# Kernel tuning notes

Measured on AMD Instinct MI355X. Metric: run time of the kernel, lower is better.

The kernel has to match this reference:

```python
import jax, jax.numpy as jnp
import numpy as np


def setup_inputs() -> dict:
    key = jax.random.key(0)
    ks = jax.random.split(key, 13)
    B, D, H, O = 4096, 2048, 3, 1  # batch, input_dim, hidden layer count, output_dim
    f32 = jnp.float32
    scale = 1.0 / np.sqrt(D)
    return {
        "x": jax.random.normal(ks[0], (B, D), f32),
        "w_mu_h": jax.random.normal(ks[1], (H, D, D), f32) * scale,
        "w_rho_h": jax.random.normal(ks[2], (H, D, D), f32) - 5.0,  # softplus(-5) ~ small std
        "b_mu_h": jax.random.normal(ks[3], (H, D), f32) * scale,
        "b_rho_h": jax.random.normal(ks[4], (H, D), f32) - 5.0,
        "w_mu_o": jax.random.normal(ks[5], (O, D), f32) * scale,
        "w_rho_o": jax.random.normal(ks[6], (O, D), f32) - 5.0,
        "b_mu_o": jax.random.normal(ks[7], (O,), f32) * scale,
        "b_rho_o": jax.random.normal(ks[8], (O,), f32) - 5.0,
        # reparameterization noise (torch.randn_like), passed explicitly for determinism
        "eps_w_h": jax.random.normal(ks[9], (H, D, D), f32),
        "eps_b_h": jax.random.normal(ks[10], (H, D), f32),
        "eps_w_o": jax.random.normal(ks[11], (O, D), f32),
        "eps_b_o": jax.random.normal(ks[12], (O,), f32),
    }


def _vlinear(x, w_mu, w_rho, b_mu, b_rho, eps_w, eps_b):
    # weight = mu + eps * softplus(rho); F.linear(x, W, b) = x @ W.T + b
    w = w_mu + eps_w * jax.nn.softplus(w_rho)
    b = b_mu + eps_b * jax.nn.softplus(b_rho)
    return x @ w.T + b


def reference(x, w_mu_h, w_rho_h, b_mu_h, b_rho_h,
              w_mu_o, w_rho_o, b_mu_o, b_rho_o,
              eps_w_h, eps_b_h, eps_w_o, eps_b_o):
    def step(h, p):
        wm, wr, bm, br, ew, eb = p
        h = jax.nn.relu(_vlinear(h, wm, wr, bm, br, ew, eb))
        return h, None

    h, _ = jax.lax.scan(step, x, (w_mu_h, w_rho_h, b_mu_h, b_rho_h, eps_w_h, eps_b_h))
    return _vlinear(h, w_mu_o, w_rho_o, b_mu_o, b_rho_o, eps_w_o, eps_b_o)
```

## Files before the change

### kernel.cpp

```cpp
#include <hip/hip_runtime.h>

#define BB 4096
#define DD 2048

typedef float f32x4 __attribute__((ext_vector_type(4)));
typedef __bf16 bf16x8 __attribute__((ext_vector_type(8)));

typedef __attribute__((address_space(1))) unsigned int gl_u32;
typedef __attribute__((address_space(3))) unsigned int lds_u32;

#define GLOAD_LDS16(gptr, sptr) \
  __builtin_amdgcn_global_load_lds((gl_u32*)(void*)(gptr), (lds_u32*)(sptr), 16, 0, 0)

#define SBAR_MEM() asm volatile("s_barrier" ::: "memory")
#define VMCNT(n)   asm volatile("s_waitcnt vmcnt(" #n ")" ::: "memory")
#define LGKMCNT0() asm volatile("s_waitcnt lgkmcnt(0)" ::: "memory")

__device__ __forceinline__ unsigned short f2bf(float f) {
  unsigned int u = __float_as_uint(f);
  u += 0x7fffu + ((u >> 16) & 1u);
  return (unsigned short)(u >> 16);
}

__device__ __forceinline__ float sp(float x) {
  float t = __expf(-fabsf(x));
  return fmaxf(x, 0.0f) + __logf(1.0f + t);
}

__device__ __forceinline__ void prep_w_vec4(
    const float* __restrict__ mu, const float* __restrict__ rho,
    const float* __restrict__ eps, unsigned short* __restrict__ Wh,
    long long i)
{
  float4 m = ((const float4*)mu)[i];
  float4 r = ((const float4*)rho)[i];
  float4 e = ((const float4*)eps)[i];
  ushort4 o;
  o.x = f2bf(m.x + e.x * sp(r.x));
  o.y = f2bf(m.y + e.y * sp(r.y));
  o.z = f2bf(m.z + e.z * sp(r.z));
  o.w = f2bf(m.w + e.w * sp(r.w));
  ((ushort4*)Wh)[i] = o;
}

__device__ __forceinline__ void prep_f32_vec4(
    const float* __restrict__ mu, const float* __restrict__ rho,
    const float* __restrict__ eps, float* __restrict__ out, long long i)
{
  float4 m = ((const float4*)mu)[i];
  float4 r = ((const float4*)rho)[i];
  float4 e = ((const float4*)eps)[i];
  float4 o;
  o.x = m.x + e.x * sp(r.x);
  o.y = m.y + e.y * sp(r.y);
  o.z = m.z + e.z * sp(r.z);
  o.w = m.w + e.w * sp(r.w);
  ((float4*)out)[i] = o;
}

__global__ __launch_bounds__(512) void prep0_kernel(
    const float* __restrict__ x,
    const float* __restrict__ wmuh, const float* __restrict__ wrhoh,
    const float* __restrict__ bmuh, const float* __restrict__ brhoh,
    const float* __restrict__ wmuo, const float* __restrict__ wrhoo,
    const float* __restrict__ epswh, const float* __restrict__ epsbh,
    const float* __restrict__ epswo,
    unsigned short* __restrict__ Wh, unsigned short* __restrict__ Xb,
    float* __restrict__ bh, float* __restrict__ wo)
{
  const int b = blockIdx.x;
  const int t = threadIdx.x;
  if (b < 1536) {
    long long base = (long long)b * 2048 + t;
    #pragma unroll
    for (int j = 0; j < 4; ++j)
      prep_w_vec4(wmuh, wrhoh, epswh, Wh, base + j * 512);
    return;
  }
  if (b < 2560) {
    long long base = (long long)(b - 1536) * 2048 + t;
    #pragma unroll
    for (int j = 0; j < 4; ++j) {
      float4 v = ((const float4*)x)[base + j * 512];
      ushort4 o;
      o.x = f2bf(v.x); o.y = f2bf(v.y); o.z = f2bf(v.z); o.w = f2bf(v.w);
      ((ushort4*)Xb)[base + j * 512] = o;
    }
    return;
  }
  #pragma unroll
  for (int j = 0; j < 3; ++j)
    prep_f32_vec4(bmuh, brhoh, epsbh, bh, j * 512 + t);
  prep_f32_vec4(wmuo, wrhoo, epswo, wo, t);
}

#define NGEMM 256

struct Coords256 { int m0, n0; int srow[4], sgc[4]; };

__device__ __forceinline__ Coords256 coords256(int id, int t) {
  Coords256 g;
  const int p = id & 7;
  const int i4 = id >> 3;
  const int mt = (p & 3) * 4 + (i4 & 3);
  const int nt = (p >> 2) * 8 + (i4 >> 2);
  g.m0 = mt * 256;
  g.n0 = nt * 128;
  #pragma unroll
  for (int i = 0; i < 4; ++i) {
    int c = i * 512 + t;
    g.srow[i] = c >> 3;
    g.sgc[i] = (c & 7) ^ (g.srow[i] & 7);
  }
  return g;
}

__device__ __forceinline__ void stage_half0(
    const unsigned short* __restrict__ A, const unsigned short* __restrict__ W,
    unsigned short* bufA, unsigned short* bufB,
    const Coords256& gc, int kt, int t)
{
  #pragma unroll
  for (int i = 0; i < 2; ++i) {
    int c = i * 512 + t;
    const unsigned short* ga = A + (size_t)(gc.m0 + gc.srow[i]) * DD + kt + gc.sgc[i] * 8;
    GLOAD_LDS16(ga, &bufA[c * 8]);
  }
  const unsigned short* gb = W + (size_t)(gc.n0 + gc.srow[0]) * DD + kt + gc.sgc[0] * 8;
  GLOAD_LDS16(gb, &bufB[t * 8]);
}

__device__ __forceinline__ void stage_half1(
    const unsigned short* __restrict__ A, const unsigned short* __restrict__ W,
    unsigned short* bufA, unsigned short* bufB,
    const Coords256& gc, int kt, int t)
{
  #pragma unroll
  for (int i = 2; i < 4; ++i) {
    int c = i * 512 + t;
    const unsigned short* ga = A + (size_t)(gc.m0 + gc.srow[i]) * DD + kt + gc.sgc[i] * 8;
    GLOAD_LDS16(ga, &bufA[c * 8]);
  }
  const unsigned short* gb = W + (size_t)(gc.n0 + gc.srow[1]) * DD + kt + gc.sgc[1] * 8;
  GLOAD_LDS16(gb, &bufB[(512 + t) * 8]);
}

__device__ __forceinline__ void compute_half(
    const unsigned short* bufA, const unsigned short* bufB, int s,
    int wm, int wn, int lq, int lr, f32x4 (&acc)[4][4])
{
  bf16x8 af[4], bfv[4];
  const int g = s * 4 + lq;
  const int go = (g ^ (lr & 7)) * 8;
  #pragma unroll
  for (int i = 0; i < 4; ++i) {
    int ra = wm * 64 + i * 16 + lr;
    af[i] = *(const bf16x8*)&bufA[ra * 64 + go];
  }
  #pragma unroll
  for (int j = 0; j < 4; ++j) {
    int rb = wn * 64 + j * 16 + lr;
    bfv[j] = *(const bf16x8*)&bufB[rb * 64 + go];
  }
  LGKMCNT0();
  __builtin_amdgcn_sched_barrier(0);
  __builtin_amdgcn_s_setprio(1);
  #pragma unroll
  for (int i = 0; i < 4; ++i)
    #pragma unroll
    for (int j = 0; j < 4; ++j)
      acc[i][j] = __builtin_amdgcn_mfma_f32_16x16x32_bf16(af[i], bfv[j], acc[i][j], 0, 0, 0);
  __builtin_amdgcn_s_setprio(0);
}

__device__ __forceinline__ void gemm_mainloop8p(
    const unsigned short* __restrict__ A, const unsigned short* __restrict__ W,
    unsigned short (*ldsA)[16384], unsigned short (*ldsB)[8192],
    const Coords256& gc, int t, f32x4 (&acc)[4][4])
{
  const int l = t & 63, lq = l >> 4, lr = l & 15;
  const int w = t >> 6, wm = w & 3, wn = w >> 2;
  unsigned short *a0 = ldsA[0], *a1 = ldsA[1], *a2 = ldsA[2];
  unsigned short *b0 = ldsB[0], *b1 = ldsB[1], *b2 = ldsB[2];
  stage_half0(A, W, a0, b0, gc, 0, t);
  stage_half1(A, W, a0, b0, gc, 0, t);
  stage_half0(A, W, a1, b1, gc, 64, t);
  stage_half1(A, W, a1, b1, gc, 64, t);
  for (int k = 0; k < 32; ++k) {
    if (k < 30) stage_half0(A, W, a2, b2, gc, (k + 2) * 64, t);
    __builtin_amdgcn_sched_barrier(0);
    if (k < 30)      { VMCNT(9); }
    else if (k == 30){ VMCNT(6); }
    else             { VMCNT(0); }
    SBAR_MEM();
    compute_half(a0, b0, 0, wm, wn, lq, lr, acc);
    SBAR_MEM();
    if (k < 30) stage_half1(A, W, a2, b2, gc, (k + 2) * 64, t);
    compute_half(a0, b0, 1, wm, wn, lq, lr, acc);
    SBAR_MEM();
    unsigned short* ta = a0; a0 = a1; a1 = a2; a2 = ta;
    unsigned short* tb = b0; b0 = b1; b1 = b2; b2 = tb;
  }
}

__device__ __forceinline__ void epilogue_store256(
    const Coords256& gc, int t, f32x4 (&acc)[4][4],
    const float* __restrict__ bias, unsigned short* __restrict__ C)
{
  const int l = t & 63, lq = l >> 4, lr = l & 15;
  const int w = t >> 6, wm = w & 3, wn = w >> 2;
  #pragma unroll
  for (int j = 0; j < 4; ++j) {
    int n = gc.n0 + wn * 64 + j * 16 + lr;
    float bv = bias[n];
    #pragma unroll
    for (int i = 0; i < 4; ++i) {
      int mbase = gc.m0 + wm * 64 + i * 16 + lq * 4;
      #pragma unroll
      for (int r = 0; r < 4; ++r) {
        float v = fmaxf(acc[i][j][r] + bv, 0.0f);
        C[(size_t)(mbase + r) * DD + n] = f2bf(v);
      }
    }
  }
}

__global__ __launch_bounds__(512, 2) void gemm_relu_kernel(
    const unsigned short* __restrict__ A,
    const unsigned short* __restrict__ W,
    const float* __restrict__ bias,
    unsigned short* __restrict__ C)
{
  __shared__ unsigned short ldsA[3][16384];
  __shared__ unsigned short ldsB[3][8192];
  const int t = threadIdx.x;
  Coords256 gc = coords256(blockIdx.x, t);
  f32x4 acc[4][4] = {};
  gemm_mainloop8p(A, W, ldsA, ldsB, gc, t, acc);
  epilogue_store256(gc, t, acc, bias, C);
}

__global__ __launch_bounds__(512, 2) void gemm_relu_dot_kernel(
    const unsigned short* __restrict__ A,
    const unsigned short* __restrict__ W,
    const float* __restrict__ bias,
    const float* __restrict__ wo,
    float* __restrict__ Pbuf)
{
  __shared__ unsigned short ldsA[3][16384];
  __shared__ unsigned short ldsB[3][8192];
  const int t = threadIdx.x;

  Coords256 gc = coords256(blockIdx.x, t);
  f32x4 acc[4][4] = {};
  gemm_mainloop8p(A, W, ldsA, ldsB, gc, t, acc);

  const int l = t & 63, lq = l >> 4, lr = l & 15;
  const int w = t >> 6, wm = w & 3, wn = w >> 2;

  float bv[4], wv[4];
  #pragma unroll
  for (int j = 0; j < 4; ++j) {
    int n = gc.n0 + wn * 64 + j * 16 + lr;
    bv[j] = bias[n];
    wv[j] = wo[n];
  }
  float partial[4][4];
  #pragma unroll
  for (int i = 0; i < 4; ++i)
    #pragma unroll
    for (int r = 0; r < 4; ++r) {
      float s = 0.0f;
      #pragma unroll
      for (int j = 0; j < 4; ++j)
        s += fmaxf(acc[i][j][r] + bv[j], 0.0f) * wv[j];
      partial[i][r] = s;
    }

  #pragma unroll
  for (int d = 1; d <= 8; d <<= 1)
    #pragma unroll
    for (int i = 0; i < 4; ++i)
      #pragma unroll
      for (int r = 0; r < 4; ++r)
        partial[i][r] += __shfl_xor(partial[i][r], d, 64);

  float* sRed = (float*)ldsA;
  if (lr == 0) {
    #pragma unroll
    for (int i = 0; i < 4; ++i)
      #pragma unroll
      for (int r = 0; r < 4; ++r) {
        int row = wm * 64 + i * 16 + lq * 4 + r;
        sRed[row * 2 + wn] = partial[i][r];
      }
  }
  __syncthreads();
  if (t < 256) {
    float s = sRed[t * 2 + 0] + sRed[t * 2 + 1];
    int nt = gc.n0 >> 7;
    Pbuf[nt * BB + gc.m0 + t] = s;
  }
}

__global__ __launch_bounds__(256) void reduce_out_kernel(
    const float* __restrict__ Pbuf,
    const float* __restrict__ bmuo, const float* __restrict__ brhoo,
    const float* __restrict__ epsbo,
    float* __restrict__ out)
{
  const int m = blockIdx.x * 256 + threadIdx.x;
  float s = bmuo[0] + epsbo[0] * sp(brhoo[0]);
  #pragma unroll
  for (int nt = 0; nt < 16; ++nt)
    s += Pbuf[nt * BB + m];
  out[m] = s;
}

extern "C" void kernel_launch(void* const* d_in, const int* in_sizes, int n_in,
                              void* d_out, int out_size, void* d_ws, size_t ws_size,
                              hipStream_t stream) {
  const float* x     = (const float*)d_in[0];
  const float* wmuh  = (const float*)d_in[1];
  const float* wrhoh = (const float*)d_in[2];
  const float* bmuh  = (const float*)d_in[3];
  const float* brhoh = (const float*)d_in[4];
  const float* wmuo  = (const float*)d_in[5];
  const float* wrhoo = (const float*)d_in[6];
  const float* bmuo  = (const float*)d_in[7];
  const float* brhoo = (const float*)d_in[8];
  const float* epswh = (const float*)d_in[9];
  const float* epsbh = (const float*)d_in[10];
  const float* epswo = (const float*)d_in[11];
  const float* epsbo = (const float*)d_in[12];

  char* ws = (char*)d_ws;
  unsigned short* Wh = (unsigned short*)(ws);
  unsigned short* Xb = (unsigned short*)(ws + 25165824);
  unsigned short* Ha = (unsigned short*)(ws + 25165824 + 16777216);
  unsigned short* Hb = (unsigned short*)(ws + 25165824 + 2 * 16777216);
  float* bh   = (float*)(ws + 25165824 + 3 * 16777216);
  float* wo   = (float*)(ws + 25165824 + 3 * 16777216 + 24576);
  float* Pbuf = (float*)(ws + 25165824 + 3 * 16777216 + 24576 + 8192);

  prep0_kernel<<<2561, 512, 0, stream>>>(
      x, wmuh, wrhoh, bmuh, brhoh, wmuo, wrhoo,
      epswh, epsbh, epswo, Wh, Xb, bh, wo);

  gemm_relu_kernel<<<NGEMM, 512, 0, stream>>>(Xb, Wh, bh, Ha);

  gemm_relu_kernel<<<NGEMM, 512, 0, stream>>>(Ha, Wh + 1 * 4194304, bh + DD, Hb);

  gemm_relu_dot_kernel<<<NGEMM, 512, 0, stream>>>(
      Hb, Wh + 2 * 4194304, bh + 2 * DD, wo, Pbuf);

  reduce_out_kernel<<<BB / 256, 256, 0, stream>>>(
      Pbuf, bmuo, brhoo, epsbo, (float*)d_out);
}
```

Measured before the change: 335.5 us.

## Restructure GEMM main loop to read both K-halves before MFMAs, drop mid barrier

The GEMM main loop now waits on the current stage once, reads LDS fragments for both K halves up front, issues the next-stage global-to-LDS loads between the reads, then runs all 32 MFMAs. The explicit lgkmcnt wait, the sched barrier and one of the workgroup barriers per iteration are removed, so the compiler can overlap LDS reads with MFMAs and there are fewer sync points. The prep kernel also batches all of its global loads before computing, to raise memory-level parallelism. The cost is higher register pressure from holding twice as many fragments, and relying on the compiler to insert the correct LDS waits.

Result: faster. 306.5 us (-8.6%).

```diff
diff --git a/kernel.cpp b/kernel.cpp
--- a/kernel.cpp
+++ b/kernel.cpp
@@ -14,7 +14,6 @@
 
 #define SBAR_MEM() asm volatile("s_barrier" ::: "memory")
 #define VMCNT(n)   asm volatile("s_waitcnt vmcnt(" #n ")" ::: "memory")
-#define LGKMCNT0() asm volatile("s_waitcnt lgkmcnt(0)" ::: "memory")
 
 __device__ __forceinline__ unsigned short f2bf(float f) {
   unsigned int u = __float_as_uint(f);
@@ -25,22 +24,6 @@
 __device__ __forceinline__ float sp(float x) {
   float t = __expf(-fabsf(x));
   return fmaxf(x, 0.0f) + __logf(1.0f + t);
-}
-
-__device__ __forceinline__ void prep_w_vec4(
-    const float* __restrict__ mu, const float* __restrict__ rho,
-    const float* __restrict__ eps, unsigned short* __restrict__ Wh,
-    long long i)
-{
-  float4 m = ((const float4*)mu)[i];
-  float4 r = ((const float4*)rho)[i];
-  float4 e = ((const float4*)eps)[i];
-  ushort4 o;
-  o.x = f2bf(m.x + e.x * sp(r.x));
-  o.y = f2bf(m.y + e.y * sp(r.y));
-  o.z = f2bf(m.z + e.z * sp(r.z));
-  o.w = f2bf(m.w + e.w * sp(r.w));
-  ((ushort4*)Wh)[i] = o;
 }
 
 __device__ __forceinline__ void prep_f32_vec4(
@@ -72,18 +55,34 @@
   const int t = threadIdx.x;
   if (b < 1536) {
     long long base = (long long)b * 2048 + t;
-    #pragma unroll
-    for (int j = 0; j < 4; ++j)
-      prep_w_vec4(wmuh, wrhoh, epswh, Wh, base + j * 512);
+    float4 m[4], r[4], e[4];
+    #pragma unroll
+    for (int j = 0; j < 4; ++j) m[j] = ((const float4*)wmuh)[base + j * 512];
+    #pragma unroll
+    for (int j = 0; j < 4; ++j) r[j] = ((const float4*)wrhoh)[base + j * 512];
+    #pragma unroll
+    for (int j = 0; j < 4; ++j) e[j] = ((const float4*)epswh)[base + j * 512];
+    #pragma unroll
+    for (int j = 0; j < 4; ++j) {
+      ushort4 o;
+      o.x = f2bf(m[j].x + e[j].x * sp(r[j].x));
+      o.y = f2bf(m[j].y + e[j].y * sp(r[j].y));
+      o.z = f2bf(m[j].z + e[j].z * sp(r[j].z));
+      o.w = f2bf(m[j].w + e[j].w * sp(r[j].w));
+      ((ushort4*)Wh)[base + j * 512] = o;
+    }
     return;
   }
   if (b < 2560) {
     long long base = (long long)(b - 1536) * 2048 + t;
+    float4 v[4];
+    #pragma unroll
+    for (int j = 0; j < 4; ++j) v[j] = ((const float4*)x)[base + j * 512];
     #pragma unroll
     for (int j = 0; j < 4; ++j) {
-      float4 v = ((const float4*)x)[base + j * 512];
       ushort4 o;
-      o.x = f2bf(v.x); o.y = f2bf(v.y); o.z = f2bf(v.z); o.w = f2bf(v.w);
+      o.x = f2bf(v[j].x); o.y = f2bf(v[j].y);
+      o.z = f2bf(v[j].z); o.w = f2bf(v[j].w);
       ((ushort4*)Xb)[base + j * 512] = o;
     }
     return;
@@ -145,35 +144,33 @@
   GLOAD_LDS16(gb, &bufB[(512 + t) * 8]);
 }
 
-__device__ __forceinline__ void compute_half(
+__device__ __forceinline__ void read_frags(
     const unsigned short* bufA, const unsigned short* bufB, int s,
-    int wm, int wn, int lq, int lr, f32x4 (&acc)[4][4])
-{
-  bf16x8 af[4], bfv[4];
+    int wm, int wn, int lq, int lr, bf16x8 (&af)[4], bf16x8 (&bv)[4])
+{
   const int g = s * 4 + lq;
   const int go = (g ^ (lr & 7)) * 8;
   #pragma unroll
-  for (int i = 0; i < 4; ++i) {
-    int ra = wm * 64 + i * 16 + lr;
-    af[i] = *(const bf16x8*)&bufA[ra * 64 + go];
-  }
-  #pragma unroll
-  for (int j = 0; j < 4; ++j) {
-    int rb = wn * 64 + j * 16 + lr;
-    bfv[j] = *(const bf16x8*)&bufB[rb * 64 + go];
-  }
-  LGKMCNT0();
-  __builtin_amdgcn_sched_barrier(0);
+  for (int i = 0; i < 4; ++i)
+    af[i] = *(const bf16x8*)&bufA[(wm * 64 + i * 16 + lr) * 64 + go];
+  #pragma unroll
+  for (int j = 0; j < 4; ++j)
+    bv[j] = *(const bf16x8*)&bufB[(wn * 64 + j * 16 + lr) * 64 + go];
+}
+
+__device__ __forceinline__ void mfma_half(
+    bf16x8 (&af)[4], bf16x8 (&bv)[4], f32x4 (&acc)[4][4])
+{
   __builtin_amdgcn_s_setprio(1);
   #pragma unroll
   for (int i = 0; i < 4; ++i)
     #pragma unroll
     for (int j = 0; j < 4; ++j)
-      acc[i][j] = __builtin_amdgcn_mfma_f32_16x16x32_bf16(af[i], bfv[j], acc[i][j], 0, 0, 0);
+      acc[i][j] = __builtin_amdgcn_mfma_f32_16x16x32_bf16(af[i], bv[j], acc[i][j], 0, 0, 0);
   __builtin_amdgcn_s_setprio(0);
 }
 
-__device__ __forceinline__ void gemm_mainloop8p(
+__device__ __forceinline__ void gemm_mainloop_fine(
     const unsigned short* __restrict__ A, const unsigned short* __restrict__ W,
     unsigned short (*ldsA)[16384], unsigned short (*ldsB)[8192],
     const Coords256& gc, int t, f32x4 (&acc)[4][4])
@@ -187,16 +184,16 @@
   stage_half0(A, W, a1, b1, gc, 64, t);
   stage_half1(A, W, a1, b1, gc, 64, t);
   for (int k = 0; k < 32; ++k) {
+    if (k < 31) { VMCNT(6); }
+    else        { VMCNT(0); }
+    SBAR_MEM();
+    bf16x8 a0f[4], b0f[4], a1f[4], b1f[4];
+    read_frags(a0, b0, 0, wm, wn, lq, lr, a0f, b0f);
     if (k < 30) stage_half0(A, W, a2, b2, gc, (k + 2) * 64, t);
-    __builtin_amdgcn_sched_barrier(0);
-    if (k < 30)      { VMCNT(9); }
-    else if (k == 30){ VMCNT(6); }
-    else             { VMCNT(0); }
-    SBAR_MEM();
-    compute_half(a0, b0, 0, wm, wn, lq, lr, acc);
-    SBAR_MEM();
+    read_frags(a0, b0, 1, wm, wn, lq, lr, a1f, b1f);
     if (k < 30) stage_half1(A, W, a2, b2, gc, (k + 2) * 64, t);
-    compute_half(a0, b0, 1, wm, wn, lq, lr, acc);
+    mfma_half(a0f, b0f, acc);
+    mfma_half(a1f, b1f, acc);
     SBAR_MEM();
     unsigned short* ta = a0; a0 = a1; a1 = a2; a2 = ta;
     unsigned short* tb = b0; b0 = b1; b1 = b2; b2 = tb;
@@ -236,7 +233,7 @@
   const int t = threadIdx.x;
   Coords256 gc = coords256(blockIdx.x, t);
   f32x4 acc[4][4] = {};
-  gemm_mainloop8p(A, W, ldsA, ldsB, gc, t, acc);
+  gemm_mainloop_fine(A, W, ldsA, ldsB, gc, t, acc);
   epilogue_store256(gc, t, acc, bias, C);
 }
 
@@ -253,7 +250,7 @@
 
   Coords256 gc = coords256(blockIdx.x, t);
   f32x4 acc[4][4] = {};
-  gemm_mainloop8p(A, W, ldsA, ldsB, gc, t, acc);
+  gemm_mainloop_fine(A, W, ldsA, ldsB, gc, t, acc);
 
   const int l = t & 63, lq = l >> 4, lr = l & 15;
   const int w = t >> 6, wm = w & 3, wn = w >> 2;
```
